# Optimization experiments

Measured on AMD Instinct MI355X. Metric: run time of the kernel, lower is better.

The kernel has to match this reference:

```python
import jax, jax.numpy as jnp
import numpy as np

EMBED_DIM = 1024
NUM_HEADS = 16
HEAD_DIM = EMBED_DIM // NUM_HEADS
NEG_INF = -1e9


def setup_inputs() -> dict:
    key = jax.random.key(0)
    k1, k2, k3, k4, k5 = jax.random.split(key, 5)
    # ragged batch: 8 segments, alternating lengths 1024 / 512 -> 6144 tokens
    lengths = np.array([1024, 512, 1024, 512, 1024, 512, 1024, 512], dtype=np.int32)
    cu_seqlens = np.concatenate([[0], np.cumsum(lengths)]).astype(np.int32)
    total = int(cu_seqlens[-1])  # 6144
    scale = 0.02
    return {
        "hidden_states": jax.random.normal(k1, (total, EMBED_DIM), dtype=jnp.float32),
        "proj_weight": jax.random.normal(k2, (3 * EMBED_DIM, EMBED_DIM), dtype=jnp.float32) * scale,
        "proj_bias": jax.random.normal(k3, (3 * EMBED_DIM,), dtype=jnp.float32) * scale,
        "out_weight": jax.random.normal(k4, (EMBED_DIM, EMBED_DIM), dtype=jnp.float32) * scale,
        "out_bias": jax.random.normal(k5, (EMBED_DIM,), dtype=jnp.float32) * scale,
        "cu_seqlens": jnp.asarray(cu_seqlens),
        "max_len": 1024,
    }


def reference(hidden_states, proj_weight, proj_bias, out_weight, out_bias, cu_seqlens, max_len):
    T = hidden_states.shape[0]
    B = cu_seqlens.shape[0] - 1
    H, Dh = NUM_HEADS, HEAD_DIM
    softmax_scale = 1.0 / jnp.sqrt(jnp.float32(Dh))

    # fused QKV projection: [T, 3E] -> [T, H, 3, Dh]
    qkv = hidden_states @ proj_weight.T + proj_bias
    qkv = qkv.reshape(T, H, 3, Dh)
    q, k, v = qkv[:, :, 0], qkv[:, :, 1], qkv[:, :, 2]  # each [T, H, Dh]

    # unpack ragged tokens into padded [B, S, H, Dh]
    lengths = cu_seqlens[1:] - cu_seqlens[:-1]            # [B]
    pos = jnp.arange(max_len)                              # [S]
    valid = pos[None, :] < lengths[:, None]                # [B, S]
    idx = jnp.where(valid, cu_seqlens[:-1, None] + pos[None, :], 0)  # [B, S]
    qp, kp, vp = q[idx], k[idx], v[idx]                    # [B, S, H, Dh]

    # per-segment attention (non-causal encoder self-attn)
    scores = jnp.einsum("bqhd,bkhd->bhqk", qp, kp) * softmax_scale  # [B,H,S,S]
    scores = jnp.where(valid[:, None, None, :], scores, NEG_INF)
    probs = jax.nn.softmax(scores, axis=-1)
    ctx = jnp.einsum("bhqk,bkhd->bqhd", probs, vp)         # [B, S, H, Dh]

    # pack back to ragged [T, E]; invalid slots scattered out-of-bounds (dropped)
    scatter_idx = jnp.where(valid, idx, T).reshape(-1)     # [B*S]
    ctx_flat = ctx.reshape(B * max_len, H * Dh)
    context = jnp.zeros((T, H * Dh), dtype=ctx_flat.dtype).at[scatter_idx].set(
        ctx_flat, mode="drop")

    return context @ out_weight.T + out_bias
```

## Files before the change

### kernel.cpp

```cpp
#include <hip/hip_runtime.h>
#include <math.h>

#define EMBED 1024
#define NHEAD 16
#define HDIM 64
#define QKV_LD 3072

typedef _Float16 f16x8 __attribute__((ext_vector_type(8)));
typedef float f32x4 __attribute__((ext_vector_type(4)));
typedef unsigned short ushort8v __attribute__((ext_vector_type(8)));
typedef unsigned short ushort4v __attribute__((ext_vector_type(4)));

__device__ __forceinline__ void gload16(const void* g, void* l) {
    __builtin_amdgcn_global_load_lds(
        (const __attribute__((address_space(1))) unsigned int*)g,
        (__attribute__((address_space(3))) unsigned int*)l, 16, 0, 0);
}

__device__ __forceinline__ int xcd_swz(int bid, int nwg) {
    int cpx = nwg >> 3;
    return (bid & 7) * cpx + (bid >> 3);
}

__device__ __forceinline__ int swz(int row, int col) {
    return row * 72 + (col ^ (((row >> 3) & 7) << 3));
}

__global__ __launch_bounds__(256) void cvt_f32_f16(
    const float* __restrict__ x, _Float16* __restrict__ y, int n4)
{
    int i = blockIdx.x * 256 + threadIdx.x;
    if (i >= n4) return;
    float4 v = reinterpret_cast<const float4*>(x)[i];
    unsigned short h0 = __builtin_bit_cast(unsigned short, (_Float16)v.x);
    unsigned short h1 = __builtin_bit_cast(unsigned short, (_Float16)v.y);
    unsigned short h2 = __builtin_bit_cast(unsigned short, (_Float16)v.z);
    unsigned short h3 = __builtin_bit_cast(unsigned short, (_Float16)v.w);
    reinterpret_cast<ushort4*>(y)[i] = make_ushort4(h0, h1, h2, h3);
}

template <bool F16_OUT>
__global__ __launch_bounds__(256) void gemm_m97(
    const _Float16* __restrict__ A, const _Float16* __restrict__ B,
    const float* __restrict__ bias, float* __restrict__ Cf,
    _Float16* __restrict__ Ch, int M, int N, int K, int gx)
{
    __shared__ __align__(16) unsigned short sA[128 * 64];
    __shared__ __align__(16) unsigned short sB[128 * 64];

    const int nwg = gridDim.x;
    const int wgid = xcd_swz(blockIdx.x, nwg);
    const int row0 = (wgid / gx) * 128;
    const int col0 = (wgid % gx) * 128;

    const int tid = threadIdx.x;
    const int lane = tid & 63;
    const int w = tid >> 6;
    const int wr = w >> 1;
    const int wc = w & 1;
    const int c = lane & 15;
    const int g = lane >> 4;

    const unsigned short* Au = (const unsigned short*)A;
    const unsigned short* Bu = (const unsigned short*)B;

    f32x4 acc[4][4];
    #pragma unroll
    for (int m = 0; m < 4; m++)
        #pragma unroll
        for (int n = 0; n < 4; n++)
            acc[m][n] = (f32x4){0.f, 0.f, 0.f, 0.f};

    size_t aoff[4], boff[4];
    int ldst[4];
    #pragma unroll
    for (int i = 0; i < 4; i++) {
        int chunk = (i * 4 + w) * 64 + lane;
        int row = chunk >> 3;
        int scol = ((chunk & 7) ^ (row & 7)) * 8;
        aoff[i] = (size_t)min(row0 + row, M - 1) * K + scol;
        boff[i] = (size_t)min(col0 + row, N - 1) * K + scol;
        ldst[i] = chunk * 8;
    }

    for (int k0 = 0; k0 < K; k0 += 64) {
        __syncthreads();
        #pragma unroll
        for (int i = 0; i < 4; i++) {
            gload16(Au + aoff[i] + k0, &sA[ldst[i]]);
            gload16(Bu + boff[i] + k0, &sB[ldst[i]]);
        }
        __syncthreads();

        #pragma unroll
        for (int ks = 0; ks < 2; ks++) {
            f16x8 af[4], bf[4];
            #pragma unroll
            for (int m = 0; m < 4; m++) {
                int row = wr * 64 + m * 16 + c;
                int cc = (ks * 4 + g) ^ (row & 7);
                af[m] = __builtin_bit_cast(f16x8, *reinterpret_cast<const ushort8v*>(
                            &sA[row * 64 + cc * 8]));
            }
            #pragma unroll
            for (int n = 0; n < 4; n++) {
                int row = wc * 64 + n * 16 + c;
                int cc = (ks * 4 + g) ^ (row & 7);
                bf[n] = __builtin_bit_cast(f16x8, *reinterpret_cast<const ushort8v*>(
                            &sB[row * 64 + cc * 8]));
            }
            #pragma unroll
            for (int m = 0; m < 4; m++)
                #pragma unroll
                for (int n = 0; n < 4; n++)
                    acc[m][n] = __builtin_amdgcn_mfma_f32_16x16x32_f16(af[m], bf[n], acc[m][n], 0, 0, 0);
        }
    }

    #pragma unroll
    for (int m = 0; m < 4; m++) {
        #pragma unroll
        for (int n = 0; n < 4; n++) {
            int cc = col0 + wc * 64 + n * 16 + c;
            if (cc >= N) continue;
            float bv = bias[cc];
            #pragma unroll
            for (int j = 0; j < 4; j++) {
                int r = row0 + wr * 64 + m * 16 + g * 4 + j;
                if (r >= M) continue;
                float v = acc[m][n][j] + bv;
                if constexpr (F16_OUT) {
                    Ch[(size_t)r * N + cc] = (_Float16)v;
                } else {
                    Cf[(size_t)r * N + cc] = v;
                }
            }
        }
    }
}

__global__ __launch_bounds__(256) void attn_mfma(
    const _Float16* __restrict__ qkv, const int* __restrict__ cu,
    _Float16* __restrict__ ctx, int B, int maxTiles)
{
    __shared__ __align__(16) unsigned short sK[64 * 72];
    __shared__ __align__(16) unsigned short sV[64 * 72];
    __shared__ __align__(16) unsigned short sP[64 * 72];

    const int nwg = gridDim.x;
    const int wgid = xcd_swz(blockIdx.x, nwg);
    const int h = wgid / maxTiles;
    const int tile = wgid % maxTiles;

    int b = -1, q0 = 0, accum = 0;
    for (int i = 0; i < B; i++) {
        int len = cu[i + 1] - cu[i];
        int nt = (len + 63) >> 6;
        if (tile < accum + nt) { b = i; q0 = (tile - accum) << 6; break; }
        accum += nt;
    }
    if (b < 0) return;
    const int s0 = cu[b];
    const int L = cu[b + 1] - s0;
    if (q0 >= L) return;

    const int tid = threadIdx.x;
    const int lane = tid & 63;
    const int w = tid >> 6;
    const int g = lane >> 4;
    const int c = lane & 15;
    const size_t qcol = (size_t)h * 192;
    const unsigned short* qkvu = (const unsigned short*)qkv;

    f16x8 q[2];
    {
        int qrow = min(q0 + w * 16 + c, L - 1);
        size_t off = (size_t)(s0 + qrow) * QKV_LD + qcol + g * 8;
        q[0] = *reinterpret_cast<const f16x8*>(&qkv[off]);
        q[1] = *reinterpret_cast<const f16x8*>(&qkv[off + 32]);
    }

    f32x4 o[4];
    #pragma unroll
    for (int n = 0; n < 4; n++) o[n] = (f32x4){0.f, 0.f, 0.f, 0.f};
    float m_r = -INFINITY;
    float l_r = 0.f;

    for (int kc = 0; kc < L; kc += 64) {
        __syncthreads();
        #pragma unroll
        for (int it = 0; it < 2; it++) {
            int idx = it * 256 + tid;
            int r = idx >> 3;
            int d0 = (idx & 7) * 8;
            int gr = min(kc + r, L - 1);
            size_t off = (size_t)(s0 + gr) * QKV_LD + qcol + 64 + d0;
            *reinterpret_cast<uint4*>(&sK[swz(r, d0)]) = *reinterpret_cast<const uint4*>(&qkvu[off]);
            ushort8v vv = *reinterpret_cast<const ushort8v*>(&qkvu[off + 64]);
            #pragma unroll
            for (int j = 0; j < 8; j++)
                sV[swz(d0 + j, r)] = vv[j];
        }
        __syncthreads();

        __builtin_amdgcn_s_setprio(1);
        f32x4 sacc[4];
        #pragma unroll
        for (int f = 0; f < 4; f++) sacc[f] = (f32x4){0.f, 0.f, 0.f, 0.f};
        #pragma unroll
        for (int f = 0; f < 4; f++) {
            #pragma unroll
            for (int ks = 0; ks < 2; ks++) {
                f16x8 kf = __builtin_bit_cast(f16x8, *reinterpret_cast<const ushort8v*>(
                               &sK[swz(f * 16 + c, ks * 32 + g * 8)]));
                sacc[f] = __builtin_amdgcn_mfma_f32_16x16x32_f16(kf, q[ks], sacc[f], 0, 0, 0);
            }
        }
        __builtin_amdgcn_s_setprio(0);

        float mx = -INFINITY;
        #pragma unroll
        for (int f = 0; f < 4; f++) {
            #pragma unroll
            for (int j = 0; j < 4; j++) {
                float v = sacc[f][j] * 0.125f;
                if (kc + f * 16 + g * 4 + j >= L) v = -1.0e9f;
                sacc[f][j] = v;
                mx = fmaxf(mx, v);
            }
        }
        mx = fmaxf(mx, __shfl_xor(mx, 16));
        mx = fmaxf(mx, __shfl_xor(mx, 32));
        float mn = fmaxf(m_r, mx);
        float fs = __expf(m_r - mn);
        float rs = 0.f;
        #pragma unroll
        for (int f = 0; f < 4; f++) {
            unsigned short hv[4];
            #pragma unroll
            for (int j = 0; j < 4; j++) {
                float p = __expf(sacc[f][j] - mn);
                rs += p;
                hv[j] = __builtin_bit_cast(unsigned short, (_Float16)p);
            }
            *reinterpret_cast<ushort4v*>(&sP[swz(w * 16 + c, f * 16 + g * 4)]) =
                (ushort4v){hv[0], hv[1], hv[2], hv[3]};
        }
        rs += __shfl_xor(rs, 16);
        rs += __shfl_xor(rs, 32);
        l_r = l_r * fs + rs;
        m_r = mn;

        #pragma unroll
        for (int j = 0; j < 4; j++) {
            float fq = __shfl(fs, (lane & 48) | (g * 4 + j));
            #pragma unroll
            for (int n = 0; n < 4; n++)
                o[n][j] *= fq;
        }

        f16x8 pa[2];
        #pragma unroll
        for (int ks = 0; ks < 2; ks++)
            pa[ks] = __builtin_bit_cast(f16x8, *reinterpret_cast<const ushort8v*>(
                         &sP[swz(w * 16 + c, ks * 32 + g * 8)]));
        __builtin_amdgcn_s_setprio(1);
        #pragma unroll
        for (int n = 0; n < 4; n++) {
            #pragma unroll
            for (int ks = 0; ks < 2; ks++) {
                f16x8 vf = __builtin_bit_cast(f16x8, *reinterpret_cast<const ushort8v*>(
                               &sV[swz(n * 16 + c, ks * 32 + g * 8)]));
                o[n] = __builtin_amdgcn_mfma_f32_16x16x32_f16(pa[ks], vf, o[n], 0, 0, 0);
            }
        }
        __builtin_amdgcn_s_setprio(0);
    }

    float linv[4];
    {
        float il = 1.0f / l_r;
        #pragma unroll
        for (int j = 0; j < 4; j++)
            linv[j] = __shfl(il, (lane & 48) | (g * 4 + j));
    }
    #pragma unroll
    for (int n = 0; n < 4; n++) {
        #pragma unroll
        for (int j = 0; j < 4; j++) {
            int r = q0 + w * 16 + g * 4 + j;
            if (r >= L) continue;
            ctx[(size_t)(s0 + r) * EMBED + h * HDIM + n * 16 + c] =
                (_Float16)(o[n][j] * linv[j]);
        }
    }
}

extern "C" void kernel_launch(void* const* d_in, const int* in_sizes, int n_in,
                              void* d_out, int out_size, void* d_ws, size_t ws_size,
                              hipStream_t stream) {
    const float* hs = (const float*)d_in[0];
    const float* pw = (const float*)d_in[1];
    const float* pb = (const float*)d_in[2];
    const float* ow = (const float*)d_in[3];
    const float* ob = (const float*)d_in[4];
    const int*   cu = (const int*)d_in[5];

    const int T = in_sizes[0] / EMBED;
    const int B = in_sizes[5] - 1;

    char* p = (char*)d_ws;
    size_t hsF_b  = (size_t)T * EMBED * sizeof(_Float16);
    size_t pwF_b  = (size_t)3 * EMBED * EMBED * sizeof(_Float16);
    size_t owF_b  = (size_t)EMBED * EMBED * sizeof(_Float16);
    size_t qkvF_b = (size_t)T * QKV_LD * sizeof(_Float16);
    size_t ctxF_b = hsF_b;

    _Float16* hsF  = (_Float16*)p;  p += hsF_b;
    _Float16* pwF  = (_Float16*)p;  p += pwF_b;
    _Float16* owF  = (_Float16*)p;  p += owF_b;
    _Float16* qkvF = (_Float16*)p;  p += qkvF_b;
    _Float16* ctxF = (_Float16*)p;  p += ctxF_b;

    float* out = (float*)d_out;
    dim3 blk(256);

    {
        int n4 = T * EMBED / 4;
        cvt_f32_f16<<<(n4 + 255) / 256, blk, 0, stream>>>(hs, hsF, n4);
        n4 = 3 * EMBED * EMBED / 4;
        cvt_f32_f16<<<(n4 + 255) / 256, blk, 0, stream>>>(pw, pwF, n4);
        n4 = EMBED * EMBED / 4;
        cvt_f32_f16<<<(n4 + 255) / 256, blk, 0, stream>>>(ow, owF, n4);
    }

    {
        int gx = (3 * EMBED) / 128;
        int nwg = gx * ((T + 127) / 128);
        gemm_m97<true><<<nwg, blk, 0, stream>>>(hsF, pwF, pb,
                                                (float*)nullptr, qkvF,
                                                T, 3 * EMBED, EMBED, gx);
    }

    {
        int maxTiles = T / 64 + B;
        int nwg = NHEAD * maxTiles;
        attn_mfma<<<nwg, blk, 0, stream>>>(qkvF, cu, ctxF, B, maxTiles);
    }

    {
        int gx = EMBED / 128;
        int nwg = gx * ((T + 127) / 128);
        gemm_m97<false><<<nwg, blk, 0, stream>>>(ctxF, owF, ob,
                                                 out, (_Float16*)nullptr,
                                                 T, EMBED, EMBED, gx);
    }
}
```

Before: 179.0 us.

## Pre-transpose V, register-prefetch K/V tiles, use exp2 softmax in attention

```diff
diff --git a/kernel.cpp b/kernel.cpp
--- a/kernel.cpp
+++ b/kernel.cpp
@@ -5,6 +5,7 @@
 #define NHEAD 16
 #define HDIM 64
 #define QKV_LD 3072
+#define SM_SCALE_LOG2 0.18033688f
 
 typedef _Float16 f16x8 __attribute__((ext_vector_type(8)));
 typedef float f32x4 __attribute__((ext_vector_type(4)));
@@ -139,9 +140,46 @@
     }
 }
 
+__global__ __launch_bounds__(256) void transpose_v(
+    const _Float16* __restrict__ qkv, _Float16* __restrict__ vT, int T, int TP)
+{
+    __shared__ __align__(16) unsigned short s[64 * 72];
+    const int nt = TP >> 6;
+    const int h = blockIdx.x / nt;
+    const int tt = blockIdx.x % nt;
+    const int tid = threadIdx.x;
+    const unsigned short* qu = (const unsigned short*)qkv;
+    unsigned short* vu = (unsigned short*)vT;
+
+    #pragma unroll
+    for (int it = 0; it < 2; it++) {
+        int idx = it * 256 + tid;
+        int tl = idx >> 3;
+        int d0 = (idx & 7) * 8;
+        int t = tt * 64 + tl;
+        uint4 val = make_uint4(0u, 0u, 0u, 0u);
+        if (t < T)
+            val = *reinterpret_cast<const uint4*>(&qu[(size_t)t * QKV_LD + h * 192 + 128 + d0]);
+        *reinterpret_cast<uint4*>(&s[swz(tl, d0)]) = val;
+    }
+    __syncthreads();
+    #pragma unroll
+    for (int it = 0; it < 2; it++) {
+        int idx = it * 256 + tid;
+        int d = idx >> 3;
+        int t0 = (idx & 7) * 8;
+        ushort8v o;
+        #pragma unroll
+        for (int j = 0; j < 8; j++)
+            o[j] = s[swz(t0 + j, d)];
+        *reinterpret_cast<ushort8v*>(&vu[((size_t)h * 64 + d) * TP + tt * 64 + t0]) = o;
+    }
+}
+
 __global__ __launch_bounds__(256) void attn_mfma(
-    const _Float16* __restrict__ qkv, const int* __restrict__ cu,
-    _Float16* __restrict__ ctx, int B, int maxTiles)
+    const _Float16* __restrict__ qkv, const _Float16* __restrict__ vT,
+    const int* __restrict__ cu, _Float16* __restrict__ ctx,
+    int B, int maxTiles, int TP)
 {
     __shared__ __align__(16) unsigned short sK[64 * 72];
     __shared__ __align__(16) unsigned short sV[64 * 72];
@@ -171,6 +209,7 @@
     const int c = lane & 15;
     const size_t qcol = (size_t)h * 192;
     const unsigned short* qkvu = (const unsigned short*)qkv;
+    const unsigned short* vTu = (const unsigned short*)vT;
 
     f16x8 q[2];
     {
@@ -180,6 +219,30 @@
         q[1] = *reinterpret_cast<const f16x8*>(&qkv[off + 32]);
     }
 
+    const int r_ = tid >> 3;
+    const int d0_ = (tid & 7) * 8;
+    int lst[2];
+    size_t kband[2], vband[2];
+    #pragma unroll
+    for (int it = 0; it < 2; it++) {
+        int r = it * 32 + r_;
+        lst[it] = swz(r, d0_);
+        kband[it] = qcol + 64 + d0_;
+        vband[it] = ((size_t)h * 64 + r) * TP + s0 + d0_;
+    }
+
+    uint4 kreg[2], vreg[2];
+    auto issue = [&](int kc) {
+        #pragma unroll
+        for (int it = 0; it < 2; it++) {
+            int gr = min(kc + it * 32 + r_, L - 1);
+            kreg[it] = *reinterpret_cast<const uint4*>(
+                           &qkvu[(size_t)(s0 + gr) * QKV_LD + kband[it]]);
+            vreg[it] = *reinterpret_cast<const uint4*>(&vTu[vband[it] + kc]);
+        }
+    };
+    issue(0);
+
     f32x4 o[4];
     #pragma unroll
     for (int n = 0; n < 4; n++) o[n] = (f32x4){0.f, 0.f, 0.f, 0.f};
@@ -190,18 +253,11 @@
         __syncthreads();
         #pragma unroll
         for (int it = 0; it < 2; it++) {
-            int idx = it * 256 + tid;
-            int r = idx >> 3;
-            int d0 = (idx & 7) * 8;
-            int gr = min(kc + r, L - 1);
-            size_t off = (size_t)(s0 + gr) * QKV_LD + qcol + 64 + d0;
-            *reinterpret_cast<uint4*>(&sK[swz(r, d0)]) = *reinterpret_cast<const uint4*>(&qkvu[off]);
-            ushort8v vv = *reinterpret_cast<const ushort8v*>(&qkvu[off + 64]);
-            #pragma unroll
-            for (int j = 0; j < 8; j++)
-                sV[swz(d0 + j, r)] = vv[j];
+            *reinterpret_cast<uint4*>(&sK[lst[it]]) = kreg[it];
+            *reinterpret_cast<uint4*>(&sV[lst[it]]) = vreg[it];
         }
         __syncthreads();
+        if (kc + 64 < L) issue(kc + 64);
 
         __builtin_amdgcn_s_setprio(1);
         f32x4 sacc[4];
@@ -219,27 +275,39 @@
         __builtin_amdgcn_s_setprio(0);
 
         float mx = -INFINITY;
-        #pragma unroll
-        for (int f = 0; f < 4; f++) {
-            #pragma unroll
-            for (int j = 0; j < 4; j++) {
-                float v = sacc[f][j] * 0.125f;
-                if (kc + f * 16 + g * 4 + j >= L) v = -1.0e9f;
-                sacc[f][j] = v;
-                mx = fmaxf(mx, v);
+        if (kc + 64 <= L) {
+            #pragma unroll
+            for (int f = 0; f < 4; f++) {
+                #pragma unroll
+                for (int j = 0; j < 4; j++) {
+                    float v = sacc[f][j] * SM_SCALE_LOG2;
+                    sacc[f][j] = v;
+                    mx = fmaxf(mx, v);
+                }
+            }
+        } else {
+            #pragma unroll
+            for (int f = 0; f < 4; f++) {
+                #pragma unroll
+                for (int j = 0; j < 4; j++) {
+                    float v = sacc[f][j] * SM_SCALE_LOG2;
+                    if (kc + f * 16 + g * 4 + j >= L) v = -1.0e9f;
+                    sacc[f][j] = v;
+                    mx = fmaxf(mx, v);
+                }
             }
         }
         mx = fmaxf(mx, __shfl_xor(mx, 16));
         mx = fmaxf(mx, __shfl_xor(mx, 32));
         float mn = fmaxf(m_r, mx);
-        float fs = __expf(m_r - mn);
+        float fs = exp2f(m_r - mn);
         float rs = 0.f;
         #pragma unroll
         for (int f = 0; f < 4; f++) {
             unsigned short hv[4];
             #pragma unroll
             for (int j = 0; j < 4; j++) {
-                float p = __expf(sacc[f][j] - mn);
+                float p = exp2f(sacc[f][j] - mn);
                 rs += p;
                 hv[j] = __builtin_bit_cast(unsigned short, (_Float16)p);
             }
@@ -308,6 +376,7 @@
 
     const int T = in_sizes[0] / EMBED;
     const int B = in_sizes[5] - 1;
+    const int TP = ((T + 63) & ~63) + 64;
 
     char* p = (char*)d_ws;
     size_t hsF_b  = (size_t)T * EMBED * sizeof(_Float16);
@@ -315,12 +384,14 @@
     size_t owF_b  = (size_t)EMBED * EMBED * sizeof(_Float16);
     size_t qkvF_b = (size_t)T * QKV_LD * sizeof(_Float16);
     size_t ctxF_b = hsF_b;
+    size_t vT_b   = (size_t)NHEAD * 64 * TP * sizeof(_Float16);
 
     _Float16* hsF  = (_Float16*)p;  p += hsF_b;
     _Float16* pwF  = (_Float16*)p;  p += pwF_b;
     _Float16* owF  = (_Float16*)p;  p += owF_b;
     _Float16* qkvF = (_Float16*)p;  p += qkvF_b;
     _Float16* ctxF = (_Float16*)p;  p += ctxF_b;
+    _Float16* vTF  = (_Float16*)p;  p += vT_b;
 
     float* out = (float*)d_out;
     dim3 blk(256);
@@ -343,9 +414,14 @@
     }
 
     {
+        int nwg = NHEAD * (TP / 64);
+        transpose_v<<<nwg, blk, 0, stream>>>(qkvF, vTF, T, TP);
+    }
+
+    {
         int maxTiles = T / 64 + B;
         int nwg = NHEAD * maxTiles;
-        attn_mfma<<<nwg, blk, 0, stream>>>(qkvF, cu, ctxF, B, maxTiles);
+        attn_mfma<<<nwg, blk, 0, stream>>>(qkvF, vTF, cu, ctxF, B, maxTiles, TP);
     }
 
     {
```

Result: slower. 225.7 us (+26.1%).

## Process 128 queries per attention block and skip lazy softmax rescaling

Applied to the files above, without the earlier changes.

```diff
diff --git a/kernel.cpp b/kernel.cpp
--- a/kernel.cpp
+++ b/kernel.cpp
@@ -5,6 +5,7 @@
 #define NHEAD 16
 #define HDIM 64
 #define QKV_LD 3072
+#define SM_SCALE_LOG2 0.18033688f
 
 typedef _Float16 f16x8 __attribute__((ext_vector_type(8)));
 typedef float f32x4 __attribute__((ext_vector_type(4)));
@@ -145,7 +146,7 @@
 {
     __shared__ __align__(16) unsigned short sK[64 * 72];
     __shared__ __align__(16) unsigned short sV[64 * 72];
-    __shared__ __align__(16) unsigned short sP[64 * 72];
+    __shared__ __align__(16) unsigned short sP[128 * 72];
 
     const int nwg = gridDim.x;
     const int wgid = xcd_swz(blockIdx.x, nwg);
@@ -155,8 +156,8 @@
     int b = -1, q0 = 0, accum = 0;
     for (int i = 0; i < B; i++) {
         int len = cu[i + 1] - cu[i];
-        int nt = (len + 63) >> 6;
-        if (tile < accum + nt) { b = i; q0 = (tile - accum) << 6; break; }
+        int nt = (len + 127) >> 7;
+        if (tile < accum + nt) { b = i; q0 = (tile - accum) << 7; break; }
         accum += nt;
     }
     if (b < 0) return;
@@ -172,19 +173,23 @@
     const size_t qcol = (size_t)h * 192;
     const unsigned short* qkvu = (const unsigned short*)qkv;
 
-    f16x8 q[2];
-    {
-        int qrow = min(q0 + w * 16 + c, L - 1);
+    f16x8 q[2][2];
+    #pragma unroll
+    for (int qa = 0; qa < 2; qa++) {
+        int qrow = min(q0 + qa * 64 + w * 16 + c, L - 1);
         size_t off = (size_t)(s0 + qrow) * QKV_LD + qcol + g * 8;
-        q[0] = *reinterpret_cast<const f16x8*>(&qkv[off]);
-        q[1] = *reinterpret_cast<const f16x8*>(&qkv[off + 32]);
-    }
-
-    f32x4 o[4];
+        q[qa][0] = *reinterpret_cast<const f16x8*>(&qkv[off]);
+        q[qa][1] = *reinterpret_cast<const f16x8*>(&qkv[off + 32]);
+    }
+
+    f32x4 o0[4], o1[4];
     #pragma unroll
-    for (int n = 0; n < 4; n++) o[n] = (f32x4){0.f, 0.f, 0.f, 0.f};
-    float m_r = -INFINITY;
-    float l_r = 0.f;
+    for (int n = 0; n < 4; n++) {
+        o0[n] = (f32x4){0.f, 0.f, 0.f, 0.f};
+        o1[n] = (f32x4){0.f, 0.f, 0.f, 0.f};
+    }
+    float m0 = -INFINITY, l0 = 0.f;
+    float m1 = -INFINITY, l1 = 0.f;
 
     for (int kc = 0; kc < L; kc += 64) {
         __syncthreads();
@@ -195,7 +200,8 @@
             int d0 = (idx & 7) * 8;
             int gr = min(kc + r, L - 1);
             size_t off = (size_t)(s0 + gr) * QKV_LD + qcol + 64 + d0;
-            *reinterpret_cast<uint4*>(&sK[swz(r, d0)]) = *reinterpret_cast<const uint4*>(&qkvu[off]);
+            *reinterpret_cast<uint4*>(&sK[swz(r, d0)]) =
+                *reinterpret_cast<const uint4*>(&qkvu[off]);
             ushort8v vv = *reinterpret_cast<const ushort8v*>(&qkvu[off + 64]);
             #pragma unroll
             for (int j = 0; j < 8; j++)
@@ -204,66 +210,128 @@
         __syncthreads();
 
         __builtin_amdgcn_s_setprio(1);
-        f32x4 sacc[4];
-        #pragma unroll
-        for (int f = 0; f < 4; f++) sacc[f] = (f32x4){0.f, 0.f, 0.f, 0.f};
+        f32x4 sa[4], sb[4];
+        #pragma unroll
+        for (int f = 0; f < 4; f++) {
+            sa[f] = (f32x4){0.f, 0.f, 0.f, 0.f};
+            sb[f] = (f32x4){0.f, 0.f, 0.f, 0.f};
+        }
         #pragma unroll
         for (int f = 0; f < 4; f++) {
             #pragma unroll
             for (int ks = 0; ks < 2; ks++) {
                 f16x8 kf = __builtin_bit_cast(f16x8, *reinterpret_cast<const ushort8v*>(
                                &sK[swz(f * 16 + c, ks * 32 + g * 8)]));
-                sacc[f] = __builtin_amdgcn_mfma_f32_16x16x32_f16(kf, q[ks], sacc[f], 0, 0, 0);
+                sa[f] = __builtin_amdgcn_mfma_f32_16x16x32_f16(kf, q[0][ks], sa[f], 0, 0, 0);
+                sb[f] = __builtin_amdgcn_mfma_f32_16x16x32_f16(kf, q[1][ks], sb[f], 0, 0, 0);
             }
         }
         __builtin_amdgcn_s_setprio(0);
 
-        float mx = -INFINITY;
-        #pragma unroll
-        for (int f = 0; f < 4; f++) {
-            #pragma unroll
-            for (int j = 0; j < 4; j++) {
-                float v = sacc[f][j] * 0.125f;
-                if (kc + f * 16 + g * 4 + j >= L) v = -1.0e9f;
-                sacc[f][j] = v;
-                mx = fmaxf(mx, v);
-            }
-        }
-        mx = fmaxf(mx, __shfl_xor(mx, 16));
-        mx = fmaxf(mx, __shfl_xor(mx, 32));
-        float mn = fmaxf(m_r, mx);
-        float fs = __expf(m_r - mn);
-        float rs = 0.f;
-        #pragma unroll
-        for (int f = 0; f < 4; f++) {
-            unsigned short hv[4];
-            #pragma unroll
-            for (int j = 0; j < 4; j++) {
-                float p = __expf(sacc[f][j] - mn);
-                rs += p;
-                hv[j] = __builtin_bit_cast(unsigned short, (_Float16)p);
-            }
-            *reinterpret_cast<ushort4v*>(&sP[swz(w * 16 + c, f * 16 + g * 4)]) =
-                (ushort4v){hv[0], hv[1], hv[2], hv[3]};
-        }
-        rs += __shfl_xor(rs, 16);
-        rs += __shfl_xor(rs, 32);
-        l_r = l_r * fs + rs;
-        m_r = mn;
-
-        #pragma unroll
-        for (int j = 0; j < 4; j++) {
-            float fq = __shfl(fs, (lane & 48) | (g * 4 + j));
-            #pragma unroll
-            for (int n = 0; n < 4; n++)
-                o[n][j] *= fq;
-        }
-
-        f16x8 pa[2];
-        #pragma unroll
-        for (int ks = 0; ks < 2; ks++)
-            pa[ks] = __builtin_bit_cast(f16x8, *reinterpret_cast<const ushort8v*>(
-                         &sP[swz(w * 16 + c, ks * 32 + g * 8)]));
+        const bool interior = (kc + 64 <= L);
+
+        {
+            float mx = -INFINITY;
+            #pragma unroll
+            for (int f = 0; f < 4; f++) {
+                #pragma unroll
+                for (int j = 0; j < 4; j++) {
+                    float v = sa[f][j] * SM_SCALE_LOG2;
+                    if (!interior && (kc + f * 16 + g * 4 + j >= L)) v = -1.0e9f;
+                    sa[f][j] = v;
+                    mx = fmaxf(mx, v);
+                }
+            }
+            mx = fmaxf(mx, __shfl_xor(mx, 16));
+            mx = fmaxf(mx, __shfl_xor(mx, 32));
+            const bool nskip = !__all(mx - m0 <= 8.0f);
+            const float mn = nskip ? fmaxf(m0, mx) : m0;
+            float rs = 0.f;
+            #pragma unroll
+            for (int f = 0; f < 4; f++) {
+                unsigned short hv[4];
+                #pragma unroll
+                for (int j = 0; j < 4; j++) {
+                    float p = exp2f(sa[f][j] - mn);
+                    rs += p;
+                    hv[j] = __builtin_bit_cast(unsigned short, (_Float16)p);
+                }
+                *reinterpret_cast<ushort4v*>(&sP[swz(w * 16 + c, f * 16 + g * 4)]) =
+                    (ushort4v){hv[0], hv[1], hv[2], hv[3]};
+            }
+            rs += __shfl_xor(rs, 16);
+            rs += __shfl_xor(rs, 32);
+            if (nskip) {
+                float fs = exp2f(m0 - mn);
+                l0 = l0 * fs + rs;
+                m0 = mn;
+                #pragma unroll
+                for (int j = 0; j < 4; j++) {
+                    float fq = __shfl(fs, (lane & 48) | (g * 4 + j));
+                    #pragma unroll
+                    for (int n = 0; n < 4; n++)
+                        o0[n][j] *= fq;
+                }
+            } else {
+                l0 += rs;
+            }
+        }
+
+        {
+            float mx = -INFINITY;
+            #pragma unroll
+            for (int f = 0; f < 4; f++) {
+                #pragma unroll
+                for (int j = 0; j < 4; j++) {
+                    float v = sb[f][j] * SM_SCALE_LOG2;
+                    if (!interior && (kc + f * 16 + g * 4 + j >= L)) v = -1.0e9f;
+                    sb[f][j] = v;
+                    mx = fmaxf(mx, v);
+                }
+            }
+            mx = fmaxf(mx, __shfl_xor(mx, 16));
+            mx = fmaxf(mx, __shfl_xor(mx, 32));
+            const bool nskip = !__all(mx - m1 <= 8.0f);
+            const float mn = nskip ? fmaxf(m1, mx) : m1;
+            float rs = 0.f;
+            #pragma unroll
+            for (int f = 0; f < 4; f++) {
+                unsigned short hv[4];
+                #pragma unroll
+                for (int j = 0; j < 4; j++) {
+                    float p = exp2f(sb[f][j] - mn);
+                    rs += p;
+                    hv[j] = __builtin_bit_cast(unsigned short, (_Float16)p);
+                }
+                *reinterpret_cast<ushort4v*>(&sP[swz(64 + w * 16 + c, f * 16 + g * 4)]) =
+                    (ushort4v){hv[0], hv[1], hv[2], hv[3]};
+            }
+            rs += __shfl_xor(rs, 16);
+            rs += __shfl_xor(rs, 32);
+            if (nskip) {
+                float fs = exp2f(m1 - mn);
+                l1 = l1 * fs + rs;
+                m1 = mn;
+                #pragma unroll
+                for (int j = 0; j < 4; j++) {
+                    float fq = __shfl(fs, (lane & 48) | (g * 4 + j));
+                    #pragma unroll
+                    for (int n = 0; n < 4; n++)
+                        o1[n][j] *= fq;
+                }
+            } else {
+                l1 += rs;
+            }
+        }
+
+        f16x8 pa0[2], pa1[2];
+        #pragma unroll
+        for (int ks = 0; ks < 2; ks++) {
+            pa0[ks] = __builtin_bit_cast(f16x8, *reinterpret_cast<const ushort8v*>(
+                          &sP[swz(w * 16 + c, ks * 32 + g * 8)]));
+            pa1[ks] = __builtin_bit_cast(f16x8, *reinterpret_cast<const ushort8v*>(
+                          &sP[swz(64 + w * 16 + c, ks * 32 + g * 8)]));
+        }
         __builtin_amdgcn_s_setprio(1);
         #pragma unroll
         for (int n = 0; n < 4; n++) {
@@ -271,27 +339,39 @@
             for (int ks = 0; ks < 2; ks++) {
                 f16x8 vf = __builtin_bit_cast(f16x8, *reinterpret_cast<const ushort8v*>(
                                &sV[swz(n * 16 + c, ks * 32 + g * 8)]));
-                o[n] = __builtin_amdgcn_mfma_f32_16x16x32_f16(pa[ks], vf, o[n], 0, 0, 0);
+                o0[n] = __builtin_amdgcn_mfma_f32_16x16x32_f16(pa0[ks], vf, o0[n], 0, 0, 0);
+                o1[n] = __builtin_amdgcn_mfma_f32_16x16x32_f16(pa1[ks], vf, o1[n], 0, 0, 0);
             }
         }
         __builtin_amdgcn_s_setprio(0);
     }
 
-    float linv[4];
-    {
-        float il = 1.0f / l_r;
-        #pragma unroll
-        for (int j = 0; j < 4; j++)
-            linv[j] = __shfl(il, (lane & 48) | (g * 4 + j));
-    }
-    #pragma unroll
-    for (int n = 0; n < 4; n++) {
+    {
+        float il = 1.0f / l0;
         #pragma unroll
         for (int j = 0; j < 4; j++) {
+            float lv = __shfl(il, (lane & 48) | (g * 4 + j));
             int r = q0 + w * 16 + g * 4 + j;
-            if (r >= L) continue;
-            ctx[(size_t)(s0 + r) * EMBED + h * HDIM + n * 16 + c] =
-                (_Float16)(o[n][j] * linv[j]);
+            if (r < L) {
+                #pragma unroll
+                for (int n = 0; n < 4; n++)
+                    ctx[(size_t)(s0 + r) * EMBED + h * HDIM + n * 16 + c] =
+                        (_Float16)(o0[n][j] * lv);
+            }
+        }
+    }
+    {
+        float il = 1.0f / l1;
+        #pragma unroll
+        for (int j = 0; j < 4; j++) {
+            float lv = __shfl(il, (lane & 48) | (g * 4 + j));
+            int r = q0 + 64 + w * 16 + g * 4 + j;
+            if (r < L) {
+                #pragma unroll
+                for (int n = 0; n < 4; n++)
+                    ctx[(size_t)(s0 + r) * EMBED + h * HDIM + n * 16 + c] =
+                        (_Float16)(o1[n][j] * lv);
+            }
         }
     }
 }
@@ -343,7 +423,7 @@
     }
 
     {
-        int maxTiles = T / 64 + B;
+        int maxTiles = T / 128 + B;
         int nwg = NHEAD * maxTiles;
         attn_mfma<<<nwg, blk, 0, stream>>>(qkvF, cu, ctxF, B, maxTiles);
     }
```

After: 200.4 us. +12.0%, slower.

## Keep softmax P in registers, use exp2, skip lazy rescale and masking

Applied to the files above, without the earlier changes.

```diff
diff --git a/kernel.cpp b/kernel.cpp
--- a/kernel.cpp
+++ b/kernel.cpp
@@ -5,6 +5,7 @@
 #define NHEAD 16
 #define HDIM 64
 #define QKV_LD 3072
+#define SM_SCALE_LOG2 0.18033688f
 
 typedef _Float16 f16x8 __attribute__((ext_vector_type(8)));
 typedef float f32x4 __attribute__((ext_vector_type(4)));
@@ -145,7 +146,6 @@
 {
     __shared__ __align__(16) unsigned short sK[64 * 72];
     __shared__ __align__(16) unsigned short sV[64 * 72];
-    __shared__ __align__(16) unsigned short sP[64 * 72];
 
     const int nwg = gridDim.x;
     const int wgid = xcd_swz(blockIdx.x, nwg);
@@ -195,7 +195,8 @@
             int d0 = (idx & 7) * 8;
             int gr = min(kc + r, L - 1);
             size_t off = (size_t)(s0 + gr) * QKV_LD + qcol + 64 + d0;
-            *reinterpret_cast<uint4*>(&sK[swz(r, d0)]) = *reinterpret_cast<const uint4*>(&qkvu[off]);
+            *reinterpret_cast<uint4*>(&sK[swz(r, d0)]) =
+                *reinterpret_cast<const uint4*>(&qkvu[off]);
             ushort8v vv = *reinterpret_cast<const ushort8v*>(&qkvu[off + 64]);
             #pragma unroll
             for (int j = 0; j < 8; j++)
@@ -219,59 +220,87 @@
         __builtin_amdgcn_s_setprio(0);
 
         float mx = -INFINITY;
-        #pragma unroll
-        for (int f = 0; f < 4; f++) {
-            #pragma unroll
-            for (int j = 0; j < 4; j++) {
-                float v = sacc[f][j] * 0.125f;
-                if (kc + f * 16 + g * 4 + j >= L) v = -1.0e9f;
-                sacc[f][j] = v;
-                mx = fmaxf(mx, v);
+        if (kc + 64 <= L) {
+            #pragma unroll
+            for (int f = 0; f < 4; f++) {
+                #pragma unroll
+                for (int j = 0; j < 4; j++) {
+                    float v = sacc[f][j] * SM_SCALE_LOG2;
+                    sacc[f][j] = v;
+                    mx = fmaxf(mx, v);
+                }
+            }
+        } else {
+            #pragma unroll
+            for (int f = 0; f < 4; f++) {
+                #pragma unroll
+                for (int j = 0; j < 4; j++) {
+                    float v = sacc[f][j] * SM_SCALE_LOG2;
+                    if (kc + f * 16 + g * 4 + j >= L) v = -1.0e9f;
+                    sacc[f][j] = v;
+                    mx = fmaxf(mx, v);
+                }
             }
         }
         mx = fmaxf(mx, __shfl_xor(mx, 16));
         mx = fmaxf(mx, __shfl_xor(mx, 32));
-        float mn = fmaxf(m_r, mx);
-        float fs = __expf(m_r - mn);
+
+        const bool nskip = !__all(mx - m_r <= 8.0f);
+        const float mn = nskip ? fmaxf(m_r, mx) : m_r;
+
+        unsigned int paw[4][2];
         float rs = 0.f;
         #pragma unroll
         for (int f = 0; f < 4; f++) {
-            unsigned short hv[4];
-            #pragma unroll
-            for (int j = 0; j < 4; j++) {
-                float p = __expf(sacc[f][j] - mn);
-                rs += p;
-                hv[j] = __builtin_bit_cast(unsigned short, (_Float16)p);
-            }
-            *reinterpret_cast<ushort4v*>(&sP[swz(w * 16 + c, f * 16 + g * 4)]) =
-                (ushort4v){hv[0], hv[1], hv[2], hv[3]};
+            float p0 = exp2f(sacc[f][0] - mn);
+            float p1 = exp2f(sacc[f][1] - mn);
+            float p2 = exp2f(sacc[f][2] - mn);
+            float p3 = exp2f(sacc[f][3] - mn);
+            rs += (p0 + p1) + (p2 + p3);
+            unsigned int h0 = __builtin_bit_cast(unsigned short, (_Float16)p0);
+            unsigned int h1 = __builtin_bit_cast(unsigned short, (_Float16)p1);
+            unsigned int h2 = __builtin_bit_cast(unsigned short, (_Float16)p2);
+            unsigned int h3 = __builtin_bit_cast(unsigned short, (_Float16)p3);
+            paw[f][0] = h0 | (h1 << 16);
+            paw[f][1] = h2 | (h3 << 16);
         }
         rs += __shfl_xor(rs, 16);
         rs += __shfl_xor(rs, 32);
-        l_r = l_r * fs + rs;
-        m_r = mn;
-
-        #pragma unroll
-        for (int j = 0; j < 4; j++) {
-            float fq = __shfl(fs, (lane & 48) | (g * 4 + j));
-            #pragma unroll
-            for (int n = 0; n < 4; n++)
-                o[n][j] *= fq;
-        }
-
-        f16x8 pa[2];
-        #pragma unroll
-        for (int ks = 0; ks < 2; ks++)
-            pa[ks] = __builtin_bit_cast(f16x8, *reinterpret_cast<const ushort8v*>(
-                         &sP[swz(w * 16 + c, ks * 32 + g * 8)]));
+
+        if (nskip) {
+            float fs = exp2f(m_r - mn);
+            l_r = l_r * fs + rs;
+            m_r = mn;
+            #pragma unroll
+            for (int j = 0; j < 4; j++) {
+                float fq = __shfl(fs, (lane & 48) | (g * 4 + j));
+                #pragma unroll
+                for (int n = 0; n < 4; n++)
+                    o[n][j] *= fq;
+            }
+        } else {
+            l_r += rs;
+        }
+
         __builtin_amdgcn_s_setprio(1);
         #pragma unroll
-        for (int n = 0; n < 4; n++) {
-            #pragma unroll
-            for (int ks = 0; ks < 2; ks++) {
-                f16x8 vf = __builtin_bit_cast(f16x8, *reinterpret_cast<const ushort8v*>(
-                               &sV[swz(n * 16 + c, ks * 32 + g * 8)]));
-                o[n] = __builtin_amdgcn_mfma_f32_16x16x32_f16(pa[ks], vf, o[n], 0, 0, 0);
+        for (int ks = 0; ks < 2; ks++) {
+            uint4 pw;
+            pw.x = paw[2 * ks][0];
+            pw.y = paw[2 * ks][1];
+            pw.z = paw[2 * ks + 1][0];
+            pw.w = paw[2 * ks + 1][1];
+            f16x8 pa = __builtin_bit_cast(f16x8, pw);
+            #pragma unroll
+            for (int n = 0; n < 4; n++) {
+                uint2 lo = *reinterpret_cast<const uint2*>(
+                               &sV[swz(n * 16 + c, ks * 32 + g * 4)]);
+                uint2 hi = *reinterpret_cast<const uint2*>(
+                               &sV[swz(n * 16 + c, ks * 32 + 16 + g * 4)]);
+                uint4 vw;
+                vw.x = lo.x; vw.y = lo.y; vw.z = hi.x; vw.w = hi.y;
+                f16x8 vf = __builtin_bit_cast(f16x8, vw);
+                o[n] = __builtin_amdgcn_mfma_f32_16x16x32_f16(pa, vf, o[n], 0, 0, 0);
             }
         }
         __builtin_amdgcn_s_setprio(0);
```

Result: no change. 180.2 us (+0.7%).
